# Optimization experiments

Hardware: AMD Instinct MI355X
Metric: run time of the kernel (lower is better)

## Reference

```python
import jax, jax.numpy as jnp
import numpy as np

D_FEAT = 64          # d
N_CTX = 8192         # n
N_LAYERS = 4         # l
LMBD = 0.9
DIM = 2 * D_FEAT + 1 # 129


def _decay_matrix(n, lmbd, dtype):
    # M[i, j] = lmbd**(i-j) for j <= i <= n-1 (lower-triangular geometric decay);
    # last row (and hence M[n, n]) is zero, matching the torch loop construction.
    idx = jnp.arange(n + 1)
    diff = idx[:, None] - idx[None, :]
    M = jnp.where(diff >= 0,
                  jnp.power(jnp.asarray(lmbd, dtype), jnp.maximum(diff, 0).astype(dtype)),
                  jnp.zeros((), dtype))
    return M.at[n].set(0.0)


def setup_inputs() -> dict:
    key = jax.random.key(0)
    kz, kp, kq = jax.random.split(key, 3)
    # xavier_normal with gain 0.1 on square (DIM, DIM) weights:
    std = 0.1 * np.sqrt(2.0 / (DIM + DIM))
    Z = jax.random.normal(kz, (DIM, N_CTX + 1), dtype=jnp.float32)
    P = std * jax.random.normal(kp, (DIM, DIM), dtype=jnp.float32)
    Q = std * jax.random.normal(kq, (DIM, DIM), dtype=jnp.float32)
    return {"Z": Z, "P": P, "Q": Q}


def reference(Z, P, Q):
    n = Z.shape[1] - 1
    M = _decay_matrix(n, LMBD, Z.dtype)
    inv_n = jnp.asarray(1.0 / n, Z.dtype)

    def attn(Zc):
        # X = Z^T Q Z : (n+1, n+1)
        X = Zc.T @ Q @ Zc
        A = jax.nn.softmax(X, axis=-1)        # activation('softmax')
        # left-to-right as in torch: ((P @ Z) @ M) @ A, each (DIM, n+1)
        return Zc + inv_n * (((P @ Zc) @ M) @ A)

    for _ in range(N_LAYERS):  # mode='auto': same layer applied l times
        Z = attn(Z)
    return Z
```

## Files before the change

kernel.cpp:

```cpp
#include <hip/hip_runtime.h>

#define D 129
#define N1 8193
#define NN 8192
#define INV_N (1.0f/8192.0f)
#define WSTR 8448
#define KP 160
#define TROWS 8448
#define PSTR 8320

typedef __attribute__((ext_vector_type(8))) short bf16x8;
typedef __attribute__((ext_vector_type(4))) float f32x4;
typedef __attribute__((ext_vector_type(4))) unsigned u32x4;
typedef __attribute__((ext_vector_type(2))) unsigned u32x2;

__device__ __forceinline__ short f2bf(float x){
  unsigned u = __float_as_uint(x);
  unsigned r = (u + 0x7fffu + ((u>>16)&1u)) >> 16;
  return (short)r;
}

__device__ __forceinline__ unsigned cvtpk(float a, float b){
  unsigned r; asm("v_cvt_pk_bf16_f32 %0, %1, %2" : "=v"(r) : "v"(a), "v"(b)); return r;
}

__device__ __forceinline__ float bf2f(unsigned short v){
  return __uint_as_float(((unsigned)v)<<16);
}

#define GLOAD_LDS16(gp, lp) __builtin_amdgcn_global_load_lds( \
    (const __attribute__((address_space(1))) void*)(gp),      \
    (__attribute__((address_space(3))) void*)(lp), 16, 0, 0)

__device__ __forceinline__ int tau(int pos){
  return (pos & 96) + ((pos & 4) << 2) + ((pos & 24) >> 1) + (pos & 3);
}

__global__ void k_tr(const float* __restrict__ src, short* __restrict__ dst, int tmax){
  __shared__ float tile[129][65];
  int t0 = blockIdx.x*64, tid = threadIdx.x;
  for(int idx=tid; idx<129*64; idx+=256){
    int d = idx>>6, c = idx&63;
    tile[d][c] = (t0+c < tmax)? src[(size_t)d*N1 + t0+c] : 0.f;
  }
  __syncthreads();
  int q = tid&3, tl = tid>>2;
  int t = t0 + tl;
  short* row = dst + (size_t)t*KP;
  int s7 = t&7;
  #pragma unroll
  for(int g5=0; g5<5; g5++){
    int gi = q*5 + g5;
    bf16x8 v;
    if(gi < 16){
      #pragma unroll
      for(int u=0;u<8;u++) v[u] = f2bf(tile[gi*8+u][tl]);
      *(bf16x8*)(row + ((gi^s7)<<3)) = v;
    } else if(gi == 16){
      v[0] = f2bf(tile[128][tl]);
      #pragma unroll
      for(int u=1;u<8;u++) v[u] = 0;
      *(bf16x8*)(row + (16<<3)) = v;
    } else {
      #pragma unroll
      for(int u=0;u<8;u++) v[u] = 0;
      *(bf16x8*)(row + (gi<<3)) = v;
    }
  }
}

__global__ __launch_bounds__(512) void k_small(
    const float* __restrict__ Z, const float* __restrict__ P,
    const float* __restrict__ Q, short* __restrict__ YT,
    float* __restrict__ PZ){
  __shared__ float qs[8][132], ps[8][132];
  __shared__ float red[16*256];
  const int tid = threadIdx.x, tx = tid&255, kg = tid>>8;
  const int r0 = blockIdx.y*8;
  for(int i=tid;i<8*129;i+=512){
    int rr=i/129, cc=i-rr*129;
    float qv=0.f, pv=0.f;
    if(r0+rr<D){ qv=Q[(r0+rr)*D+cc]; pv=P[(r0+rr)*D+cc]; }
    qs[rr][cc]=qv; ps[rr][cc]=pv;
  }
  __syncthreads();
  const int t = blockIdx.x*256 + tx;
  const bool valid = (t < N1);
  const int tc = valid ? t : (N1-1);
  const float* zp = Z + tc;
  float ay[8], ap[8];
  #pragma unroll
  for(int rr=0;rr<8;rr++){ ay[rr]=0.f; ap[rr]=0.f; }
  const int kbeg = kg ? 65 : 0, kend = kg ? 129 : 65;
  for(int k=kbeg;k<kend;k++){
    float z = zp[(size_t)k*N1];
    #pragma unroll
    for(int rr=0;rr<8;rr++){
      ay[rr] = fmaf(qs[rr][k], z, ay[rr]);
      ap[rr] = fmaf(ps[rr][k], z, ap[rr]);
    }
  }
  if(kg==1){
    #pragma unroll
    for(int rr=0;rr<8;rr++){
      red[rr*256+tx]     = ay[rr];
      red[(8+rr)*256+tx] = ap[rr];
    }
  }
  __syncthreads();
  if(kg==0){
    #pragma unroll
    for(int rr=0;rr<8;rr++){
      ay[rr] += red[rr*256+tx];
      ap[rr] += red[(8+rr)*256+tx];
    }
    short* row = YT + (size_t)t*KP;
    const int s7 = t&7;
    const int gc = r0>>3;
    bf16x8 v;
    #pragma unroll
    for(int u=0;u<8;u++) v[u] = f2bf(valid ? ay[u] : 0.f);
    if(gc < 16){
      *(bf16x8*)(row + ((gc^s7)<<3)) = v;
    } else {
      *(bf16x8*)(row + (16<<3)) = v;
      bf16x8 zv;
      #pragma unroll
      for(int u=0;u<8;u++) zv[u]=0;
      *(bf16x8*)(row + (17<<3)) = zv;
      *(bf16x8*)(row + (18<<3)) = zv;
      *(bf16x8*)(row + (19<<3)) = zv;
    }
    #pragma unroll
    for(int rr=0;rr<8;rr++){
      int r=r0+rr;
      if(r<D) PZ[(size_t)r*WSTR + t] = valid ? ap[rr] : 0.f;
    }
  }
}

__global__ void k_scan(const float* __restrict__ PZ, float* __restrict__ W){
  __shared__ float s[2376];
  int d = blockIdx.y;
  int base = blockIdx.x*2048;
  for(int i=threadIdx.x;i<2304;i+=128){
    int j = base+i;
    s[i + (i>>5)] = (j<NN)? PZ[(size_t)d*WSTR + j] : 0.f;
  }
  __syncthreads();
  int t = threadIdx.x;
  int jh = t*16+15;
  float acc = 0.f, f = 1.f;
  for(int k=0;k<256;k++){ int a = jh+k; acc = fmaf(f, s[a+(a>>5)], acc); f *= 0.9f; }
  float wv[16];
  wv[15] = acc;
  #pragma unroll
  for(int r=14;r>=0;r--){ int a = t*16+r; wv[r] = fmaf(0.9f, wv[r+1], s[a+(a>>5)]); }
  float* out = W + (size_t)d*WSTR + base + t*16;
  #pragma unroll
  for(int r=0;r<16;r+=4) *(f32x4*)(out+r) = (f32x4){wv[r],wv[r+1],wv[r+2],wv[r+3]};
}

__global__ void k_ssum(const float* __restrict__ S_part, float* __restrict__ S,
                       int i_base, int count){
  int idx = blockIdx.x*256+threadIdx.x;
  if(idx>=count) return;
  int i = i_base + idx;
  float s=0.f;
  #pragma unroll 3
  for(int jtb=0;jtb<33;jtb++) s += S_part[(size_t)jtb*WSTR + i];
  S[i]=s;
}

__global__ void k_v(const float* __restrict__ W, const float* __restrict__ S,
                    short* __restrict__ Vt, int tile0){
  int idx = blockIdx.x*256+threadIdx.x;
  int l = idx/18432, rem = idx - l*18432;
  int d = rem>>7, ci = rem&127;
  int it = tile0 + l;
  int i = it*128 + tau(ci);
  float v = (d<=128)? W[(size_t)d*WSTR + i]/S[i] : 0.f;
  int gs = (ci>>3) ^ (d&7);
  Vt[(size_t)it*18432 + (d<<7) + gs*8 + (ci&7)] = f2bf(v);
}

__global__ __launch_bounds__(512,4) void k_qke(
    const short* __restrict__ ZT, const short* __restrict__ YT,
    short* __restrict__ Ebuf, float* __restrict__ S_part, int tile0, int ITC, int nwg){
  __shared__ short zt[128*KP];
  __shared__ short sp[32*132];
  const int tid=threadIdx.x, w=tid>>6, lane=tid&63, g=lane>>4, lm=lane&15;
  int bid = blockIdx.x;
  int qq = nwg>>3, rr8 = nwg&7, xcd = bid&7, ix = bid>>3;
  int wg = (xcd<rr8 ? xcd*(qq+1) : rr8*(qq+1)+(xcd-rr8)*qq) + ix;
  const int jtb = wg/ITC, itl = wg - jtb*ITC;
  const int it = tile0 + itl;
  const int sx = lm&7;

  const short* ztg = ZT + (size_t)it*(128*KP);
  #pragma unroll
  for(int q=0;q<5;q++){
    int off = (q*512 + tid)*8;
    GLOAD_LDS16(ztg + off, zt + off);
  }

  bf16x8 b[2][5];
  #pragma unroll
  for(int p=0;p<2;p++){
    int jr = jtb*256 + w*32 + p*16 + lm;
    const short* rp = YT + (size_t)jr*KP;
    #pragma unroll
    for(int kk=0;kk<4;kk++) b[p][kk] = *(const bf16x8*)(rp + (((kk*4+g)^sx)<<3));
    b[p][4] = *(const bf16x8*)(rp + ((16+g)<<3));
  }
  const int jl0 = w*32 + lm, jl1 = jl0 + 16;
  const bool jv0 = (jtb*256 + jl0) < N1;
  const bool jv1 = (jtb*256 + jl1) < N1;
  short* ep0 = Ebuf + ((size_t)(jtb*2 + (jl0>>7))*ITC + itl)*16384 + (jl0&127)*128;
  short* ep1 = Ebuf + ((size_t)(jtb*2 + (jl1>>7))*ITC + itl)*16384 + (jl1&127)*128;
  const int er0 = jl0&7, er1 = jl1&7;
  const int wl = w*4 + (lm>>2);
  __syncthreads();

  #pragma unroll
  for(int p2=0;p2<4;p2++){
    const int ib0 = 2*p2, ib1 = ib0+1;
    f32x4 aA0={0.f,0.f,0.f,0.f}, aA1={0.f,0.f,0.f,0.f};
    f32x4 aB0={0.f,0.f,0.f,0.f}, aB1={0.f,0.f,0.f,0.f};
    const short* zpA = zt + (ib0*16+lm)*KP;
    const short* zpB = zt + (ib1*16+lm)*KP;
    #pragma unroll
    for(int kk=0;kk<4;kk++){
      bf16x8 fa = *(const bf16x8*)(zpA + (((kk*4+g)^sx)<<3));
      bf16x8 fb = *(const bf16x8*)(zpB + (((kk*4+g)^sx)<<3));
      aA0 = __builtin_amdgcn_mfma_f32_16x16x32_bf16(fa, b[0][kk], aA0, 0,0,0);
      aA1 = __builtin_amdgcn_mfma_f32_16x16x32_bf16(fa, b[1][kk], aA1, 0,0,0);
      aB0 = __builtin_amdgcn_mfma_f32_16x16x32_bf16(fb, b[0][kk], aB0, 0,0,0);
      aB1 = __builtin_amdgcn_mfma_f32_16x16x32_bf16(fb, b[1][kk], aB1, 0,0,0);
    }
    {
      bf16x8 fa = *(const bf16x8*)(zpA + ((16+g)<<3));
      bf16x8 fb = *(const bf16x8*)(zpB + ((16+g)<<3));
      aA0 = __builtin_amdgcn_mfma_f32_16x16x32_bf16(fa, b[0][4], aA0, 0,0,0);
      aA1 = __builtin_amdgcn_mfma_f32_16x16x32_bf16(fa, b[1][4], aA1, 0,0,0);
      aB0 = __builtin_amdgcn_mfma_f32_16x16x32_bf16(fb, b[0][4], aB0, 0,0,0);
      aB1 = __builtin_amdgcn_mfma_f32_16x16x32_bf16(fb, b[1][4], aB1, 0,0,0);
    }
    float eA0[4], eA1[4], eB0[4], eB1[4];
    #pragma unroll
    for(int r=0;r<4;r++){
      eA0[r] = jv0 ? __expf(aA0[r]) : 0.f;
      eA1[r] = jv1 ? __expf(aA1[r]) : 0.f;
      eB0[r] = jv0 ? __expf(aB0[r]) : 0.f;
      eB1[r] = jv1 ? __expf(aB1[r]) : 0.f;
    }
    const int c0 = p2*4 + g;
    *(u32x4*)(ep0 + ((c0^er0)<<3)) =
      (u32x4){cvtpk(eA0[0],eA0[1]), cvtpk(eA0[2],eA0[3]), cvtpk(eB0[0],eB0[1]), cvtpk(eB0[2],eB0[3])};
    *(u32x4*)(ep1 + ((c0^er1)<<3)) =
      (u32x4){cvtpk(eA1[0],eA1[1]), cvtpk(eA1[2],eA1[3]), cvtpk(eB1[0],eB1[1]), cvtpk(eB1[2],eB1[3])};
    float vA[4], vB[4];
    #pragma unroll
    for(int r=0;r<4;r++){
      float sa = eA0[r] + eA1[r];
      sa += __shfl_xor(sa,1); sa += __shfl_xor(sa,2);
      vA[r]=sa;
      float sb = eB0[r] + eB1[r];
      sb += __shfl_xor(sb,1); sb += __shfl_xor(sb,2);
      vB[r]=sb;
    }
    if((lm&3)==0){
      int i0 = p2*32 + g*4;
      *(u32x2*)(sp + wl*132 + i0)      = (u32x2){cvtpk(vA[0],vA[1]), cvtpk(vA[2],vA[3])};
      *(u32x2*)(sp + wl*132 + i0 + 16) = (u32x2){cvtpk(vB[0],vB[1]), cvtpk(vB[2],vB[3])};
    }
  }
  __syncthreads();
  {
    int i = tid>>2, q = tid&3;
    float s=0.f;
    #pragma unroll
    for(int k=0;k<8;k++) s += bf2f((unsigned short)sp[(q*8+k)*132 + i]);
    s += __shfl_xor(s,1); s += __shfl_xor(s,2);
    if(q==0) S_part[(size_t)jtb*WSTR + it*128 + i] = s;
  }
}

__global__ __launch_bounds__(512) void k_pv(
    const short* __restrict__ Ebuf, const short* __restrict__ Vt,
    float* __restrict__ part, int ITC, int tile0, int ks_base, int nT){
  __shared__ short lds[2][34816];
  const int tid=threadIdx.x, w=tid>>6, lane=tid&63, g=lane>>4, lm=lane&15;
  const int jt = blockIdx.x;
  const int ks = ks_base + blockIdx.y;
  const int t0l = blockIdx.y*nT;
  const int sx = lm&7;

  f32x4 acc[9];
  #pragma unroll
  for(int m=0;m<9;m++) acc[m] = (f32x4){0.f,0.f,0.f,0.f};

  auto stage = [&](int buf, int tl){
    const short* eg = Ebuf + ((size_t)jt*ITC + tl)*16384;
    short* eb = &lds[buf][0];
    #pragma unroll
    for(int q=0;q<4;q++){
      int off = (q*512 + tid)*8;
      GLOAD_LDS16(eg + off, eb + off);
    }
    const short* vg = Vt + (size_t)(tile0 + tl)*18432;
    short* vb = &lds[buf][16384];
    #pragma unroll
    for(int q=0;q<5;q++){
      int off = (q*512 + tid)*8;
      if(q<4 || tid<256) GLOAD_LDS16(vg + off, vb + off);
    }
  };

  stage(0, t0l);
  __syncthreads();

  for(int t=0; t<nT; ++t){
    if(t+1<nT) stage((t+1)&1, t0l+t+1);
    const short* eb = &lds[t&1][0];
    const short* vb = &lds[t&1][16384];
    const short* ep = eb + (w*16+lm)*128;
    #pragma unroll
    for(int kk=0;kk<4;kk++){
      int go = ((kk*4+g)^sx)<<3;
      bf16x8 b = *(const bf16x8*)(ep + go);
      #pragma unroll
      for(int m=0;m<9;m++){
        bf16x8 av = *(const bf16x8*)(vb + ((m*16+lm)<<7) + go);
        acc[m] = __builtin_amdgcn_mfma_f32_16x16x32_bf16(av, b, acc[m], 0,0,0);
      }
    }
    __syncthreads();
  }

  float* pb = part + (size_t)ks*144*PSTR;
  const int j = jt*128 + w*16 + lm;
  #pragma unroll
  for(int m=0;m<9;m++){
    #pragma unroll
    for(int r=0;r<4;r++)
      pb[(size_t)(m*16+g*4+r)*PSTR + j] = acc[m][r];
  }
}

__global__ void k_out(const float* __restrict__ Zc, const float* __restrict__ part,
                      float* __restrict__ out, int st){
  int idx = blockIdx.x*256+threadIdx.x;
  if(idx >= 129*2049) return;
  int d = idx/2049, jq = idx - d*2049;
  int j0 = jq*4;
  float s0=0.f,s1=0.f,s2=0.f,s3=0.f;
  for(int ks=0;ks<st;ks++){
    f32x4 v = *(const f32x4*)(part + (size_t)ks*144*PSTR + (size_t)d*PSTR + j0);
    s0+=v[0]; s1+=v[1]; s2+=v[2]; s3+=v[3];
  }
  const float* zr = Zc + (size_t)d*N1;
  float* orow = out + (size_t)d*N1;
  float sv[4] = {s0,s1,s2,s3};
  #pragma unroll
  for(int u=0;u<4;u++){
    int j = j0+u;
    if(j < N1) orow[j] = zr[j] + INV_N*sv[u];
  }
}

extern "C" void kernel_launch(void* const* d_in, const int* in_sizes, int n_in,
                              void* d_out, int out_size, void* d_ws, size_t ws_size,
                              hipStream_t stream){
  (void)in_sizes; (void)n_in; (void)out_size;
  const float* Zin=(const float*)d_in[0];
  const float* Pm =(const float*)d_in[1];
  const float* Qm =(const float*)d_in[2];
  float* out=(float*)d_out;

  const size_t fixed = 2*(size_t)D*N1*4 + 2*(size_t)D*WSTR*4 + (size_t)WSTR*4
                     + (size_t)33*WSTR*4
                     + 2*(size_t)TROWS*KP*2 + (size_t)64*18432*2 + 16*4096;
  int c=8, ksPC=1;
  {
    const int cs[5] = {1,1,2,4,8};
    const int kp[5] = {8,4,2,1,1};
    for(int k=0;k<5;k++){
      int stc = cs[k]*kp[k];
      size_t need = fixed + (size_t)stc*144*PSTR*4 + (size_t)66*(64/cs[k])*16384*2;
      if(need <= ws_size){ c=cs[k]; ksPC=kp[k]; break; }
    }
  }
  const int ITC = 64/c, nT = ITC/ksPC, st = c*ksPC;

  char* base=(char*)d_ws;
  size_t off=0;
  auto alloc=[&](size_t b)->void*{ void* p=base+off; off=(off+b+255)&~(size_t)255; return p; };
  float* Z0  =(float*)alloc((size_t)D*N1*4);
  float* Z1  =(float*)alloc((size_t)D*N1*4);
  float* PZ  =(float*)alloc((size_t)D*WSTR*4);
  float* Wf  =(float*)alloc((size_t)D*WSTR*4);
  float* S   =(float*)alloc((size_t)WSTR*4);
  float* Sp  =(float*)alloc((size_t)33*WSTR*4);
  short* ZT  =(short*)alloc((size_t)TROWS*KP*2);
  short* YT  =(short*)alloc((size_t)TROWS*KP*2);
  short* Vt  =(short*)alloc((size_t)64*18432*2);
  float* part=(float*)alloc((size_t)st*144*PSTR*4);
  short* Ebuf=(short*)alloc((size_t)66*ITC*16384*2);

  const float* Zc=Zin;
  for(int l=0;l<4;l++){
    float* Zn = (l==3)? out : ((l&1)? Z1:Z0);
    k_small<<<dim3(33,17),dim3(512),0,stream>>>(Zc,Pm,Qm,YT,PZ);
    k_tr<<<dim3(132),dim3(256),0,stream>>>(Zc,ZT,N1);
    k_scan<<<dim3(4,D),dim3(128),0,stream>>>(PZ,Wf);
    for(int ch=0; ch<c; ch++){
      int tile0 = ch*ITC;
      int nwg = 33*ITC;
      k_qke<<<dim3(nwg),dim3(512),0,stream>>>(ZT,YT,Ebuf,Sp,tile0,ITC,nwg);
      k_ssum<<<dim3((ITC*128+255)/256),dim3(256),0,stream>>>(Sp,S,tile0*128,ITC*128);
      k_v<<<dim3(ITC*72),dim3(256),0,stream>>>(Wf,S,Vt,tile0);
      k_pv<<<dim3(65,ksPC),dim3(512),0,stream>>>(Ebuf,Vt,part,ITC,tile0,ch*ksPC,nT);
    }
    k_out<<<dim3(1033),dim3(256),0,stream>>>(Zc,part,Zn,st);
    Zc=Zn;
  }
}
```

Baseline: 639.7 us.

## Load E tiles directly into registers in k_pv, staging only V through LDS

The PV kernel no longer stages the exp-score (E) tile through LDS. Each lane loads its E fragment straight from global memory into registers, with a two-deep register double buffer, so only V is staged in LDS. This roughly halves LDS use per block, and a launch-bounds occupancy hint of 4 is added. The E writer drops its XOR swizzle so rows are laid out contiguously for the direct loads. The risks are longer exposed global latency on E loads and more register pressure under the occupancy hint.

```diff
diff --git a/kernel.cpp b/kernel.cpp
--- a/kernel.cpp
+++ b/kernel.cpp
@@ -218,7 +218,6 @@
   const bool jv1 = (jtb*256 + jl1) < N1;
   short* ep0 = Ebuf + ((size_t)(jtb*2 + (jl0>>7))*ITC + itl)*16384 + (jl0&127)*128;
   short* ep1 = Ebuf + ((size_t)(jtb*2 + (jl1>>7))*ITC + itl)*16384 + (jl1&127)*128;
-  const int er0 = jl0&7, er1 = jl1&7;
   const int wl = w*4 + (lm>>2);
   __syncthreads();
 
@@ -255,9 +254,9 @@
       eB1[r] = jv1 ? __expf(aB1[r]) : 0.f;
     }
     const int c0 = p2*4 + g;
-    *(u32x4*)(ep0 + ((c0^er0)<<3)) =
+    *(u32x4*)(ep0 + (c0<<3)) =
       (u32x4){cvtpk(eA0[0],eA0[1]), cvtpk(eA0[2],eA0[3]), cvtpk(eB0[0],eB0[1]), cvtpk(eB0[2],eB0[3])};
-    *(u32x4*)(ep1 + ((c0^er1)<<3)) =
+    *(u32x4*)(ep1 + (c0<<3)) =
       (u32x4){cvtpk(eA1[0],eA1[1]), cvtpk(eA1[2],eA1[3]), cvtpk(eB1[0],eB1[1]), cvtpk(eB1[2],eB1[3])};
     float vA[4], vB[4];
     #pragma unroll
@@ -286,10 +285,10 @@
   }
 }
 
-__global__ __launch_bounds__(512) void k_pv(
+__global__ __launch_bounds__(512,4) void k_pv(
     const short* __restrict__ Ebuf, const short* __restrict__ Vt,
     float* __restrict__ part, int ITC, int tile0, int ks_base, int nT){
-  __shared__ short lds[2][34816];
+  __shared__ short vlds[2][18432];
   const int tid=threadIdx.x, w=tid>>6, lane=tid&63, g=lane>>4, lm=lane&15;
   const int jt = blockIdx.x;
   const int ks = ks_base + blockIdx.y;
@@ -300,42 +299,45 @@
   #pragma unroll
   for(int m=0;m<9;m++) acc[m] = (f32x4){0.f,0.f,0.f,0.f};
 
-  auto stage = [&](int buf, int tl){
-    const short* eg = Ebuf + ((size_t)jt*ITC + tl)*16384;
-    short* eb = &lds[buf][0];
-    #pragma unroll
-    for(int q=0;q<4;q++){
-      int off = (q*512 + tid)*8;
-      GLOAD_LDS16(eg + off, eb + off);
-    }
+  auto stageV = [&](int buf, int tl){
     const short* vg = Vt + (size_t)(tile0 + tl)*18432;
-    short* vb = &lds[buf][16384];
+    short* vb = &vlds[buf][0];
     #pragma unroll
     for(int q=0;q<5;q++){
-      int off = (q*512 + tid)*8;
-      if(q<4 || tid<256) GLOAD_LDS16(vg + off, vb + off);
+      int idx = q*512 + tid;
+      if(idx < 2304) GLOAD_LDS16(vg + idx*8, vb + idx*8);
     }
   };
-
-  stage(0, t0l);
-  __syncthreads();
-
-  for(int t=0; t<nT; ++t){
-    if(t+1<nT) stage((t+1)&1, t0l+t+1);
-    const short* eb = &lds[t&1][0];
-    const short* vb = &lds[t&1][16384];
-    const short* ep = eb + (w*16+lm)*128;
+  const short* erow = Ebuf + (size_t)jt*ITC*16384 + (w*16+lm)*128 + (g<<3);
+  auto loadE = [&](bf16x8 (&e)[4], int tl){
+    const short* ep = erow + (size_t)tl*16384;
+    #pragma unroll
+    for(int kk=0;kk<4;kk++) e[kk] = *(const bf16x8*)(ep + (kk<<5));
+  };
+  auto compute = [&](int buf, bf16x8 (&e)[4]){
+    const short* vb = &vlds[buf][0];
     #pragma unroll
     for(int kk=0;kk<4;kk++){
       int go = ((kk*4+g)^sx)<<3;
-      bf16x8 b = *(const bf16x8*)(ep + go);
       #pragma unroll
       for(int m=0;m<9;m++){
         bf16x8 av = *(const bf16x8*)(vb + ((m*16+lm)<<7) + go);
-        acc[m] = __builtin_amdgcn_mfma_f32_16x16x32_bf16(av, b, acc[m], 0,0,0);
+        acc[m] = __builtin_amdgcn_mfma_f32_16x16x32_bf16(av, e[kk], acc[m], 0,0,0);
       }
     }
+  };
+
+  bf16x8 eA[4], eB[4];
+  stageV(0, t0l);
+  loadE(eA, t0l);
+
+  for(int t=0; t<nT; t+=2){
     __syncthreads();
+    if(t+1<nT){ stageV(1, t0l+t+1); loadE(eB, t0l+t+1); }
+    compute(0, eA);
+    __syncthreads();
+    if(t+2<nT){ stageV(0, t0l+t+2); loadE(eA, t0l+t+2); }
+    if(t+1<nT) compute(1, eB);
   }
 
   float* pb = part + (size_t)ks*144*PSTR;
```

Result: faster. 626.1 us (-2.1%).
